# Kernel tuning notes

Hardware: AMD Instinct MI355X
Metric: run time of the kernel (lower is better)

## Reference

```python
import jax, jax.numpy as jnp
import numpy as np

H = 16          # n_heads
WIN = 256       # window_size
NEG_INF = -1e30 # finite stand-in for -inf to stay fp16/bf16 safe


def setup_inputs() -> dict:
    key = jax.random.key(0)
    ks = jax.random.split(key, 9)
    B, L, C = 2, 2048, 2048
    s = 0.02  # weight init scale
    inp = {
        "x": jax.random.normal(ks[0], (B, L, C), jnp.float32),
        "Wq": jax.random.normal(ks[1], (C, C), jnp.float32) * s,
        "bq": jnp.zeros((C,), jnp.float32),
        "Wk": jax.random.normal(ks[2], (C, C), jnp.float32) * s,
        "bk": jnp.zeros((C,), jnp.float32),
        "Wv": jax.random.normal(ks[3], (C, C), jnp.float32) * s,
        "bv": jnp.zeros((C,), jnp.float32),
        "Wo": jax.random.normal(ks[4], (C, C), jnp.float32) * s,
        "bo": jnp.zeros((C,), jnp.float32),
    }
    return inp


def _attn(x, Wq, bq, Wk, bk, Wv, bv, Wo, bo):
    B, L, C = x.shape
    D = C // H
    # torch Linear: y = x @ W.T + b
    q = (x @ Wq.T + bq).reshape(B, L, H, D).transpose(0, 2, 1, 3)  # (B,H,L,D)
    k = (x @ Wk.T + bk).reshape(B, L, H, D).transpose(0, 2, 1, 3)
    v = (x @ Wv.T + bv).reshape(B, L, H, D).transpose(0, 2, 1, 3)
    i = jnp.arange(L)[:, None]
    j = jnp.arange(L)[None, :]
    allowed = (j <= i) & (j > i - WIN)
    bias = jnp.where(allowed, 0.0, NEG_INF).astype(x.dtype)  # (L,L)
    scale = 1.0 / np.sqrt(D)
    attn = jnp.einsum('bhid,bhjd->bhij', q, k) + bias
    a = jax.nn.softmax(attn * scale, axis=-1)
    out = jnp.einsum('bhij,bhjd->bhid', a, v)  # (B,H,L,D)
    out = out.transpose(0, 2, 1, 3).reshape(B, L, C)
    return out @ Wo.T + bo  # dropout = identity (eval mode)


def reference(x, Wq, bq, Wk, bk, Wv, bv, Wo, bo):
    return _attn(x, Wq, bq, Wk, bk, Wv, bv, Wo, bo)
```

## Files before the change

### kernel.cpp

```cpp
#include <hip/hip_runtime.h>
#include <hip/hip_bf16.h>
#include <stdint.h>

typedef __bf16 bf16;
typedef __attribute__((ext_vector_type(8))) __bf16 bf16x8;
typedef __attribute__((ext_vector_type(8))) unsigned short u16x8;
typedef __attribute__((ext_vector_type(4))) float f32x4;

#define L_SEQ 2048
#define C_DIM 2048
#define NBATCH 2
#define M_ROWS (NBATCH * L_SEQ)
#define DH 128
#define NHEAD 16
#define WINSZ 256

__device__ __forceinline__ float san(float v, float s) {
    return ((__float_as_uint(v) & 0x7f800000u) == 0x7f800000u) ? s : v;
}

__device__ __forceinline__ bf16x8 pack8(float4 lo, float4 hi) {
    bf16x8 v;
    v[0] = (bf16)lo.x; v[1] = (bf16)lo.y; v[2] = (bf16)lo.z; v[3] = (bf16)lo.w;
    v[4] = (bf16)hi.x; v[5] = (bf16)hi.y; v[6] = (bf16)hi.z; v[7] = (bf16)hi.w;
    return v;
}

typedef const __attribute__((address_space(1))) void g_void;
typedef __attribute__((address_space(3))) void l_void;
__device__ __forceinline__ void glds16(const void* g, void* l) {
    __builtin_amdgcn_global_load_lds((g_void*)g, (l_void*)l, 16, 0, 0);
}

template <bool AF32, bool OUTF32>
__global__ __launch_bounds__(256)
void gemm_bt_bias(const void* __restrict__ Ap,
                  const float* __restrict__ W0, const float* __restrict__ b0, void* O0,
                  const float* __restrict__ W1, const float* __restrict__ b1, void* O1,
                  const float* __restrict__ W2, const float* __restrict__ b2, void* O2,
                  float snt)
{
    const int K = C_DIM, N = C_DIM;
    const float* W = W0; const float* bias = b0; void* Out = O0;
    if (blockIdx.z == 1)      { W = W1; bias = b1; Out = O1; }
    else if (blockIdx.z == 2) { W = W2; bias = b2; Out = O2; }

    __shared__ bf16 As[128 * 32];
    __shared__ bf16 Bs[128 * 32];

    const int tid  = threadIdx.x;
    const int lane = tid & 63;
    const int m0 = blockIdx.x * 128;
    const int n0 = blockIdx.y * 128;

    const int wave = tid >> 6;
    const int wm = (wave >> 1) * 64;
    const int wn = (wave & 1) * 64;

    const int srow = tid >> 2;
    const int scol = (tid & 3) * 8;

    f32x4 acc[4][4] = {};

    const int fr = lane & 15;
    const int fq = (lane >> 4) * 8;

    for (int k0 = 0; k0 < K; k0 += 32) {
        bf16x8 ra[2], rb[2];
        #pragma unroll
        for (int p = 0; p < 2; p++) {
            const size_t aoff = (size_t)(m0 + p * 64 + srow) * K + k0 + scol;
            if (AF32) {
                const float* A = (const float*)Ap;
                float4 lo = *(const float4*)(A + aoff);
                float4 hi = *(const float4*)(A + aoff + 4);
                ra[p] = pack8(lo, hi);
            } else {
                const bf16* A = (const bf16*)Ap;
                ra[p] = *(const bf16x8*)(A + aoff);
            }
            const size_t boff = (size_t)(n0 + p * 64 + srow) * K + k0 + scol;
            float4 wlo = *(const float4*)(W + boff);
            float4 whi = *(const float4*)(W + boff + 4);
            rb[p] = pack8(wlo, whi);
        }
        __syncthreads();
        #pragma unroll
        for (int p = 0; p < 2; p++) {
            *(bf16x8*)&As[(p * 64 + srow) * 32 + scol] = ra[p];
            *(bf16x8*)&Bs[(p * 64 + srow) * 32 + scol] = rb[p];
        }
        __syncthreads();

        bf16x8 af[4], bfr[4];
        #pragma unroll
        for (int s = 0; s < 4; s++)
            af[s] = *(const bf16x8*)&As[(wm + s * 16 + fr) * 32 + fq];
        #pragma unroll
        for (int s = 0; s < 4; s++)
            bfr[s] = *(const bf16x8*)&Bs[(wn + s * 16 + fr) * 32 + fq];
        #pragma unroll
        for (int sm = 0; sm < 4; sm++)
            #pragma unroll
            for (int sn = 0; sn < 4; sn++)
                acc[sm][sn] = __builtin_amdgcn_mfma_f32_16x16x32_bf16(af[sm], bfr[sn], acc[sm][sn], 0, 0, 0);
    }

    const int r0 = (lane >> 4) * 4;
    const int cn = lane & 15;
    #pragma unroll
    for (int sn = 0; sn < 4; sn++) {
        const int n = n0 + wn + sn * 16 + cn;
        const float bv = bias[n];
        #pragma unroll
        for (int sm = 0; sm < 4; sm++) {
            const int m = m0 + wm + sm * 16 + r0;
            #pragma unroll
            for (int r = 0; r < 4; r++) {
                const float v = san(acc[sm][sn][r] + bv, snt);
                if (OUTF32) ((float*)Out)[(size_t)(m + r) * N + n] = v;
                else        ((bf16*)Out)[(size_t)(m + r) * N + n] = (bf16)v;
            }
        }
    }
}

__device__ __forceinline__ void phase_mid() {
    asm volatile("" ::: "memory");
    __builtin_amdgcn_s_barrier();
    asm volatile("s_waitcnt lgkmcnt(0)" ::: "memory");
    __builtin_amdgcn_sched_barrier(0);
    __builtin_amdgcn_s_setprio(1);
}
__device__ __forceinline__ void phase_end() {
    __builtin_amdgcn_s_setprio(0);
    asm volatile("" ::: "memory");
    __builtin_amdgcn_s_barrier();
}

#define LOADA(d, qm) do {                                                     \
    char* s_ = lds + (d) * 65536 + ahalf * 16384;                             \
    _Pragma("unroll") for (int sm = 0; sm < 4; sm++)                          \
    _Pragma("unroll") for (int kk = 0; kk < 2; kk++) {                        \
        const int row_ = (qm) * 64 + sm * 16 + fr;                            \
        afr[sm][kk] = *(const bf16x8*)(s_ + row_ * 128 +                      \
                        (((kk * 4 + g) ^ (row_ & 7)) << 4));                  \
    } } while (0)

#define LOADB(d, qn, arr) do {                                                \
    char* s_ = lds + (d) * 65536 + 32768 + bhalf * 16384;                     \
    _Pragma("unroll") for (int sn = 0; sn < 2; sn++)                          \
    _Pragma("unroll") for (int kk = 0; kk < 2; kk++) {                        \
        const int row_ = brow0 + (qn) * 32 + sn * 16 + fr;                    \
        arr[sn][kk] = *(const bf16x8*)(s_ + row_ * 128 +                      \
                        (((kk * 4 + g) ^ (row_ & 7)) << 4));                  \
    } } while (0)

#define MFMA16(qm, qn, arr) do {                                              \
    _Pragma("unroll") for (int kk = 0; kk < 2; kk++)                          \
    _Pragma("unroll") for (int sm = 0; sm < 4; sm++)                          \
    _Pragma("unroll") for (int sn = 0; sn < 2; sn++)                          \
        acc[(qm) * 4 + sm][(qn) * 2 + sn] =                                   \
            __builtin_amdgcn_mfma_f32_16x16x32_bf16(afr[sm][kk], arr[sn][kk], \
                acc[(qm) * 4 + sm][(qn) * 2 + sn], 0, 0, 0);                  \
    } while (0)

template <bool OUTF32>
__global__ __launch_bounds__(512, 2)
void gemm_256(const bf16* __restrict__ A,
              const bf16* __restrict__ W0, const float* __restrict__ b0, void* O0,
              const bf16* __restrict__ W1, const float* __restrict__ b1, void* O1,
              const bf16* __restrict__ W2, const float* __restrict__ b2, void* O2,
              float snt)
{
    const int K = C_DIM, N = C_DIM;
    const int NT = K / 64;
    const bf16* W = W0; const float* bias = b0; void* Out = O0;
    if (blockIdx.z == 1)      { W = W1; bias = b1; Out = O1; }
    else if (blockIdx.z == 2) { W = W2; bias = b2; Out = O2; }

    __shared__ __attribute__((aligned(16))) char lds[131072];

    const int tid  = threadIdx.x;
    const int lane = tid & 63;
    const int w    = tid >> 6;

    int id = blockIdx.x + (int)gridDim.x * blockIdx.y;
    id = (id & 7) * 16 + (id >> 3);
    const int m0 = (id & 15) * 256;
    const int n0 = (id >> 4) * 256;

    const int wm = (w >> 2) * 128;
    const int wn = (w & 3) * 64;
    const int fr = lane & 15;
    const int g  = lane >> 4;
    const int ahalf = w >> 2;
    const int bhalf = (w >> 1) & 1;
    const int brow0 = (w & 1) * 64;

    const int srow  = tid >> 3;
    const int scol  = (((tid & 7) ^ (srow & 7)) * 8);
    const int wvoff = (tid >> 6) * 1024;

    f32x4 acc[8][4] = {};
    bf16x8 afr[4][2], b0r[2][2], b1r[2][2];

    #define STAGE_A(t, h) do {                                                \
        const int d_ = (t) & 1;                                               \
        const int tc_ = (t) < NT ? (t) : NT - 1;                              \
        const bf16* src_ = A + (size_t)(m0 + (h) * 128 + srow) * K            \
                             + tc_ * 64 + scol;                               \
        char* dst_ = lds + d_ * 65536 + (h) * 16384 + wvoff;                  \
        glds16(src_, dst_);                                                   \
        glds16(src_ + (size_t)64 * K, dst_ + 8192);                           \
    } while (0)

    #define STAGE_B(t, h) do {                                                \
        const int d_ = (t) & 1;                                               \
        const int tc_ = (t) < NT ? (t) : NT - 1;                              \
        const bf16* src_ = W + (size_t)(n0 + (h) * 128 + srow) * K            \
                             + tc_ * 64 + scol;                               \
        char* dst_ = lds + d_ * 65536 + 32768 + (h) * 16384 + wvoff;          \
        glds16(src_, dst_);                                                   \
        glds16(src_ + (size_t)64 * K, dst_ + 8192);                           \
    } while (0)

    STAGE_B(0, 0); STAGE_B(0, 1); STAGE_A(0, 0); STAGE_A(0, 1);
    STAGE_B(1, 0); STAGE_B(1, 1);
    asm volatile("s_waitcnt vmcnt(4)" ::: "memory");
    asm volatile("" ::: "memory");
    __builtin_amdgcn_s_barrier();

    #pragma unroll 1
    for (int i = 0; i < NT / 2; i++) {
        const int t1 = 2 * i + 1, t2 = 2 * i + 2, t3 = 2 * i + 3;
        LOADA(0, 0); LOADB(0, 0, b0r);
        STAGE_A(t1, 0);
        phase_mid(); MFMA16(0, 0, b0r); phase_end();
        LOADB(0, 1, b1r);
        STAGE_A(t1, 1);
        phase_mid(); MFMA16(0, 1, b1r); phase_end();
        LOADA(0, 1);
        STAGE_B(t2, 0);
        phase_mid(); MFMA16(1, 1, b1r); phase_end();
        STAGE_B(t2, 1);
        asm volatile("s_waitcnt vmcnt(4)" ::: "memory");
        phase_mid(); MFMA16(1, 0, b0r); phase_end();
        LOADA(1, 0); LOADB(1, 0, b0r);
        STAGE_A(t2, 0);
        phase_mid(); MFMA16(0, 0, b0r); phase_end();
        LOADB(1, 1, b1r);
        STAGE_A(t2, 1);
        phase_mid(); MFMA16(0, 1, b1r); phase_end();
        LOADA(1, 1);
        STAGE_B(t3, 0);
        phase_mid(); MFMA16(1, 1, b1r); phase_end();
        STAGE_B(t3, 1);
        asm volatile("s_waitcnt vmcnt(4)" ::: "memory");
        phase_mid(); MFMA16(1, 0, b0r); phase_end();
    }
    asm volatile("s_waitcnt vmcnt(0)" ::: "memory");

    const int cn = lane & 15;
    const int r0 = (lane >> 4) * 4;
    #pragma unroll
    for (int sn2 = 0; sn2 < 4; sn2++) {
        const int n = n0 + wn + sn2 * 16 + cn;
        const float bv = bias[n];
        #pragma unroll
        for (int sm2 = 0; sm2 < 8; sm2++) {
            const int m = m0 + wm + sm2 * 16 + r0;
            #pragma unroll
            for (int r = 0; r < 4; r++) {
                const float v = san(acc[sm2][sn2][r] + bv, snt);
                if (OUTF32) ((float*)Out)[(size_t)(m + r) * N + n] = v;
                else        ((bf16*)Out)[(size_t)(m + r) * N + n] = (bf16)v;
            }
        }
    }
    #undef STAGE_A
    #undef STAGE_B
}

__global__ __launch_bounds__(256)
void cvt_f32_bf16(const float* __restrict__ s0, bf16* __restrict__ d0,
                  const float* __restrict__ s1, bf16* __restrict__ d1,
                  const float* __restrict__ s2, bf16* __restrict__ d2,
                  const float* __restrict__ s3, bf16* __restrict__ d3,
                  const float* __restrict__ s4, bf16* __restrict__ d4)
{
    const float* s; bf16* d; int n;
    switch (blockIdx.y) {
        case 0:  s = s0; d = d0; n = M_ROWS * C_DIM; break;
        case 1:  s = s1; d = d1; n = C_DIM * C_DIM; break;
        case 2:  s = s2; d = d2; n = C_DIM * C_DIM; break;
        case 3:  s = s3; d = d3; n = C_DIM * C_DIM; break;
        default: s = s4; d = d4; n = C_DIM * C_DIM; break;
    }
    const int nv = n >> 3;
    const int stride = (int)gridDim.x * 256;
    for (int i = blockIdx.x * 256 + threadIdx.x; i < nv; i += stride) {
        const float4 lo = *(const float4*)(s + (size_t)i * 8);
        const float4 hi = *(const float4*)(s + (size_t)i * 8 + 4);
        *(bf16x8*)(d + (size_t)i * 8) = pack8(lo, hi);
    }
}

#define SWZK(r, byteoff) ((((r) * 256) + (byteoff)) ^ (((r) & 7) << 4))
#define SWZV(d, byteoff) ((((d) * 128) + (byteoff)) ^ (((((d) & 7) ^ (((d) >> 3) & 7))) << 4))
#define SWZP(r, byteoff) ((((r) * 128) + (byteoff)) ^ (((r) & 7) << 4))

__global__ __launch_bounds__(256)
void swa_attn(const bf16* __restrict__ Q, const bf16* __restrict__ Kp,
              const bf16* __restrict__ V, bf16* __restrict__ Oattn, float snt)
{
    __shared__ bf16 Ks[64 * 128];
    __shared__ bf16 Vt[128 * 64];
    __shared__ bf16 Ps[64 * 64];

    const int tid  = threadIdx.x;
    const int lane = tid & 63;
    const int w    = tid >> 6;
    const int q0 = blockIdx.x * 64;
    const int h  = blockIdx.y;
    const int b  = blockIdx.z;
    const size_t base = (size_t)b * L_SEQ * C_DIM + (size_t)h * DH;

    const int fr  = lane & 15;
    const int g   = lane >> 4;
    const int fq8 = g * 8;

    bf16x8 qf[4];
    {
        const bf16* qrow = Q + base + (size_t)(q0 + w * 16 + fr) * C_DIM;
        #pragma unroll
        for (int kk = 0; kk < 4; kk++)
            qf[kk] = *(const bf16x8*)(qrow + kk * 32 + fq8);
    }

    const int rl0 = g * 4;
    const int ig  = q0 + w * 16 + rl0;
    const float scale = 0.08838834764831845f;

    float m_run[4], l_run[4];
    #pragma unroll
    for (int r = 0; r < 4; r++) { m_run[r] = -1e30f; l_run[r] = 0.0f; }
    f32x4 Oacc[8] = {};

    const int krr = tid >> 4;
    const int kcc = (tid & 15) * 8;
    const int vc  = tid & 15;
    const int vd0 = vc * 8;
    const int vpb = tid >> 4;

    for (int kb = 0; kb < 5; kb++) {
        const int s = q0 - 256 + kb * 64;
        if (s < 0) continue;

        __syncthreads();

        #pragma unroll
        for (int p = 0; p < 4; p++) {
            const int r = p * 16 + krr;
            const uint4 kv = *(const uint4*)(Kp + base + (size_t)(s + r) * C_DIM + kcc);
            *(uint4*)((char*)Ks + SWZK(r, kcc * 2)) = kv;
        }
        #pragma unroll
        for (int it = 0; it < 2; it++) {
            const int p = vpb + it * 16;
            const bf16* vr = V + base + (size_t)(s + 2 * p) * C_DIM + vd0;
            const u16x8 va = *(const u16x8*)vr;
            const u16x8 vb = *(const u16x8*)(vr + C_DIM);
            #pragma unroll
            for (int j = 0; j < 8; j++) {
                const uint32_t val = (uint32_t)va[j] | ((uint32_t)vb[j] << 16);
                *(uint32_t*)((char*)Vt + SWZV(vd0 + j, 4 * p)) = val;
            }
        }
        __syncthreads();

        f32x4 sacc[4] = {};
        __builtin_amdgcn_s_setprio(1);
        #pragma unroll
        for (int kk = 0; kk < 4; kk++) {
            #pragma unroll
            for (int t = 0; t < 4; t++) {
                const bf16x8 kf = *(const bf16x8*)((char*)Ks + SWZK(t * 16 + fr, (kk * 32 + fq8) * 2));
                sacc[t] = __builtin_amdgcn_mfma_f32_16x16x32_bf16(qf[kk], kf, sacc[t], 0, 0, 0);
            }
        }
        __builtin_amdgcn_s_setprio(0);

        float alpha[4];
        #pragma unroll
        for (int r = 0; r < 4; r++) {
            const int iq = ig + r;
            float p4[4];
            float bm = -1e30f;
            #pragma unroll
            for (int t = 0; t < 4; t++) {
                const int j = s + t * 16 + fr;
                const bool allow = (j <= iq) && (j > iq - WINSZ);
                p4[t] = allow ? sacc[t][r] * scale : -1e30f;
                bm = fmaxf(bm, p4[t]);
            }
            bm = fmaxf(bm, __shfl_xor(bm, 1, 64));
            bm = fmaxf(bm, __shfl_xor(bm, 2, 64));
            bm = fmaxf(bm, __shfl_xor(bm, 4, 64));
            bm = fmaxf(bm, __shfl_xor(bm, 8, 64));
            const float m_new = fmaxf(m_run[r], bm);
            alpha[r] = __expf(m_run[r] - m_new);
            m_run[r] = m_new;
            float ps = 0.0f;
            #pragma unroll
            for (int t = 0; t < 4; t++) {
                const float e = (p4[t] > -1e29f) ? __expf(p4[t] - m_new) : 0.0f;
                p4[t] = e;
                ps += e;
            }
            ps += __shfl_xor(ps, 1, 64);
            ps += __shfl_xor(ps, 2, 64);
            ps += __shfl_xor(ps, 4, 64);
            ps += __shfl_xor(ps, 8, 64);
            l_run[r] = l_run[r] * alpha[r] + ps;

            const int prow = w * 16 + rl0 + r;
            #pragma unroll
            for (int t = 0; t < 4; t++)
                *(bf16*)((char*)Ps + SWZP(prow, (t * 16 + fr) * 2)) = (bf16)p4[t];
        }

        #pragma unroll
        for (int t = 0; t < 8; t++)
            #pragma unroll
            for (int r = 0; r < 4; r++)
                Oacc[t][r] *= alpha[r];

        __builtin_amdgcn_s_setprio(1);
        #pragma unroll
        for (int kk = 0; kk < 2; kk++) {
            const bf16x8 pa = *(const bf16x8*)((char*)Ps + SWZP(w * 16 + fr, (kk * 32 + fq8) * 2));
            #pragma unroll
            for (int t = 0; t < 8; t++) {
                const bf16x8 vf = *(const bf16x8*)((char*)Vt + SWZV(t * 16 + fr, (kk * 32 + fq8) * 2));
                Oacc[t] = __builtin_amdgcn_mfma_f32_16x16x32_bf16(pa, vf, Oacc[t], 0, 0, 0);
            }
        }
        __builtin_amdgcn_s_setprio(0);
    }

    bf16* ob = Oattn + base;
    #pragma unroll
    for (int r = 0; r < 4; r++) {
        const float inv_l = 1.0f / l_run[r];
        const size_t ro = (size_t)(q0 + w * 16 + rl0 + r) * C_DIM;
        #pragma unroll
        for (int t = 0; t < 8; t++)
            ob[ro + t * 16 + fr] = (bf16)san(Oacc[t][r] * inv_l, snt);
    }
}

__global__ void fill_signal(float* out, int n, float v) {
    for (int i = blockIdx.x * blockDim.x + threadIdx.x; i < n; i += gridDim.x * blockDim.x)
        out[i] = v;
}

extern "C" void kernel_launch(void* const* d_in, const int* in_sizes, int n_in,
                              void* d_out, int out_size, void* d_ws, size_t ws_size,
                              hipStream_t stream) {
    const size_t sz      = (size_t)M_ROWS * C_DIM;
    const size_t wsz     = (size_t)C_DIM * C_DIM;
    const size_t bfbytes = sz * sizeof(bf16);
    const size_t FASTNEED = 3 * sz * sizeof(bf16) + 4 * wsz * sizeof(bf16);

    const int expn[9] = {8388608, 4194304, 2048, 4194304, 2048,
                         4194304, 2048, 4194304, 2048};
    float sig = 0.0f;
    if (n_in != 9) sig = 1100.0f;
    else {
        for (int i = 0; i < 9; i++)
            if (in_sizes[i] != expn[i]) { sig = 1200.0f + 100.0f * i; break; }
    }
    if (sig == 0.0f && out_size != (int)sz) sig = 2100.0f;
    if (sig == 0.0f && ws_size < 2 * bfbytes) sig = 3000.0f + 10.0f * (float)(ws_size >> 20);
    if (sig != 0.0f) {
        fill_signal<<<512, 256, 0, stream>>>((float*)d_out, (int)sz, sig);
        return;
    }

    const float* x  = (const float*)d_in[0];
    const float* Wq = (const float*)d_in[1];
    const float* bq = (const float*)d_in[2];
    const float* Wk = (const float*)d_in[3];
    const float* bk = (const float*)d_in[4];
    const float* Wv = (const float*)d_in[5];
    const float* bv = (const float*)d_in[6];
    const float* Wo = (const float*)d_in[7];
    const float* bo = (const float*)d_in[8];

    if (ws_size >= FASTNEED) {
        bf16* xbf = (bf16*)d_ws;
        bf16* kws = xbf + sz;
        bf16* vws = kws + sz;
        bf16* wqb = vws + sz;
        bf16* wkb = wqb + wsz;
        bf16* wvb = wkb + wsz;
        bf16* wob = wvb + wsz;
        bf16*  qscr  = (bf16*)d_out;
        float* out32 = (float*)d_out;

        cvt_f32_bf16<<<dim3(2048, 5), 256, 0, stream>>>(
            x, xbf, Wq, wqb, Wk, wkb, Wv, wvb, Wo, wob);

        gemm_256<false><<<dim3(16, 8, 3), 512, 0, stream>>>(
            xbf, wqb, bq, (void*)qscr, wkb, bk, (void*)kws,
            wvb, bv, (void*)vws, 111.0f);

        swa_attn<<<dim3(L_SEQ / 64, NHEAD, NBATCH), 256, 0, stream>>>(
            qscr, kws, vws, xbf, 222.0f);

        gemm_256<true><<<dim3(16, 8, 1), 512, 0, stream>>>(
            xbf, wob, bo, (void*)out32, wob, bo, (void*)out32,
            wob, bo, (void*)out32, 444.0f);
    } else {
        bf16*  kws   = (bf16*)d_ws;
        bf16*  vws   = kws + sz;
        bf16*  qscr  = (bf16*)d_out;
        float* out32 = (float*)d_out;

        gemm_bt_bias<true, false><<<dim3(32, 16, 3), 256, 0, stream>>>(
            (const void*)x, Wq, bq, (void*)qscr, Wk, bk, (void*)kws,
            Wv, bv, (void*)vws, 111.0f);

        swa_attn<<<dim3(L_SEQ / 64, NHEAD, NBATCH), 256, 0, stream>>>(
            qscr, kws, vws, qscr, 222.0f);

        hipMemcpyAsync(kws, qscr, bfbytes, hipMemcpyDeviceToDevice, stream);

        gemm_bt_bias<false, true><<<dim3(32, 16, 1), 256, 0, stream>>>(
            (const void*)kws, Wo, bo, (void*)out32, Wo, bo, (void*)out32,
            Wo, bo, (void*)out32, 444.0f);
    }
}
```

Before: 359.8 us.

## Shrink GEMM block tile to 256x128 to double the grid and cut LDS

```diff
diff --git a/kernel.cpp b/kernel.cpp
--- a/kernel.cpp
+++ b/kernel.cpp
@@ -138,40 +138,43 @@
     __builtin_amdgcn_s_barrier();
 }
 
-#define LOADA(d, qm) do {                                                     \
-    char* s_ = lds + (d) * 65536 + ahalf * 16384;                             \
+#define BUFSZ 49152
+#define BOFF  32768
+
+#define LDA2(d) do {                                                          \
+    char* s_ = lds + (d) * BUFSZ + ahalf * 16384;                             \
     _Pragma("unroll") for (int sm = 0; sm < 4; sm++)                          \
     _Pragma("unroll") for (int kk = 0; kk < 2; kk++) {                        \
-        const int row_ = (qm) * 64 + sm * 16 + fr;                            \
+        const int row_ = arow0 + sm * 16 + fr;                                \
         afr[sm][kk] = *(const bf16x8*)(s_ + row_ * 128 +                      \
                         (((kk * 4 + g) ^ (row_ & 7)) << 4));                  \
     } } while (0)
 
-#define LOADB(d, qn, arr) do {                                                \
-    char* s_ = lds + (d) * 65536 + 32768 + bhalf * 16384;                     \
+#define LDB2(d, qn, arr) do {                                                 \
+    char* s_ = lds + (d) * BUFSZ + BOFF;                                      \
     _Pragma("unroll") for (int sn = 0; sn < 2; sn++)                          \
     _Pragma("unroll") for (int kk = 0; kk < 2; kk++) {                        \
-        const int row_ = brow0 + (qn) * 32 + sn * 16 + fr;                    \
+        const int row_ = wn + (qn) * 32 + sn * 16 + fr;                       \
         arr[sn][kk] = *(const bf16x8*)(s_ + row_ * 128 +                      \
                         (((kk * 4 + g) ^ (row_ & 7)) << 4));                  \
     } } while (0)
 
-#define MFMA16(qm, qn, arr) do {                                              \
+#define MFMAH(qn, arr) do {                                                   \
     _Pragma("unroll") for (int kk = 0; kk < 2; kk++)                          \
     _Pragma("unroll") for (int sm = 0; sm < 4; sm++)                          \
     _Pragma("unroll") for (int sn = 0; sn < 2; sn++)                          \
-        acc[(qm) * 4 + sm][(qn) * 2 + sn] =                                   \
+        acc[sm][(qn) * 2 + sn] =                                              \
             __builtin_amdgcn_mfma_f32_16x16x32_bf16(afr[sm][kk], arr[sn][kk], \
-                acc[(qm) * 4 + sm][(qn) * 2 + sn], 0, 0, 0);                  \
+                acc[sm][(qn) * 2 + sn], 0, 0, 0);                             \
     } while (0)
 
 template <bool OUTF32>
 __global__ __launch_bounds__(512, 2)
-void gemm_256(const bf16* __restrict__ A,
-              const bf16* __restrict__ W0, const float* __restrict__ b0, void* O0,
-              const bf16* __restrict__ W1, const float* __restrict__ b1, void* O1,
-              const bf16* __restrict__ W2, const float* __restrict__ b2, void* O2,
-              float snt)
+void gemm_256x128(const bf16* __restrict__ A,
+                  const bf16* __restrict__ W0, const float* __restrict__ b0, void* O0,
+                  const bf16* __restrict__ W1, const float* __restrict__ b1, void* O1,
+                  const bf16* __restrict__ W2, const float* __restrict__ b2, void* O2,
+                  float snt)
 {
     const int K = C_DIM, N = C_DIM;
     const int NT = K / 64;
@@ -179,54 +182,52 @@
     if (blockIdx.z == 1)      { W = W1; bias = b1; Out = O1; }
     else if (blockIdx.z == 2) { W = W2; bias = b2; Out = O2; }
 
-    __shared__ __attribute__((aligned(16))) char lds[131072];
+    __shared__ __attribute__((aligned(16))) char lds[98304];
 
     const int tid  = threadIdx.x;
     const int lane = tid & 63;
     const int w    = tid >> 6;
 
     int id = blockIdx.x + (int)gridDim.x * blockIdx.y;
-    id = (id & 7) * 16 + (id >> 3);
+    id = (id & 7) * 32 + (id >> 3);
     const int m0 = (id & 15) * 256;
-    const int n0 = (id >> 4) * 256;
-
-    const int wm = (w >> 2) * 128;
-    const int wn = (w & 3) * 64;
+    const int n0 = (id >> 4) * 128;
+
+    const int wm = (w >> 1) * 64;
+    const int wn = (w & 1) * 64;
     const int fr = lane & 15;
     const int g  = lane >> 4;
     const int ahalf = w >> 2;
-    const int bhalf = (w >> 1) & 1;
-    const int brow0 = (w & 1) * 64;
+    const int arow0 = ((w >> 1) & 1) * 64;
 
     const int srow  = tid >> 3;
     const int scol  = (((tid & 7) ^ (srow & 7)) * 8);
     const int wvoff = (tid >> 6) * 1024;
 
-    f32x4 acc[8][4] = {};
+    f32x4 acc[4][4] = {};
     bf16x8 afr[4][2], b0r[2][2], b1r[2][2];
 
-    #define STAGE_A(t, h) do {                                                \
+    #define STAGE_A(t) do {                                                   \
         const int d_ = (t) & 1;                                               \
         const int tc_ = (t) < NT ? (t) : NT - 1;                              \
-        const bf16* src_ = A + (size_t)(m0 + (h) * 128 + srow) * K            \
-                             + tc_ * 64 + scol;                               \
-        char* dst_ = lds + d_ * 65536 + (h) * 16384 + wvoff;                  \
-        glds16(src_, dst_);                                                   \
+        const bf16* src_ = A + (size_t)(m0 + srow) * K + tc_ * 64 + scol;     \
+        char* dst_ = lds + d_ * BUFSZ + wvoff;                                \
+        glds16(src_,                   dst_);                                 \
+        glds16(src_ + (size_t)64 * K,  dst_ + 8192);                          \
+        glds16(src_ + (size_t)128 * K, dst_ + 16384);                         \
+        glds16(src_ + (size_t)192 * K, dst_ + 24576);                         \
+    } while (0)
+
+    #define STAGE_B(t) do {                                                   \
+        const int d_ = (t) & 1;                                               \
+        const int tc_ = (t) < NT ? (t) : NT - 1;                              \
+        const bf16* src_ = W + (size_t)(n0 + srow) * K + tc_ * 64 + scol;     \
+        char* dst_ = lds + d_ * BUFSZ + BOFF + wvoff;                         \
+        glds16(src_,                  dst_);                                  \
         glds16(src_ + (size_t)64 * K, dst_ + 8192);                           \
     } while (0)
 
-    #define STAGE_B(t, h) do {                                                \
-        const int d_ = (t) & 1;                                               \
-        const int tc_ = (t) < NT ? (t) : NT - 1;                              \
-        const bf16* src_ = W + (size_t)(n0 + (h) * 128 + srow) * K            \
-                             + tc_ * 64 + scol;                               \
-        char* dst_ = lds + d_ * 65536 + 32768 + (h) * 16384 + wvoff;          \
-        glds16(src_, dst_);                                                   \
-        glds16(src_ + (size_t)64 * K, dst_ + 8192);                           \
-    } while (0)
-
-    STAGE_B(0, 0); STAGE_B(0, 1); STAGE_A(0, 0); STAGE_A(0, 1);
-    STAGE_B(1, 0); STAGE_B(1, 1);
+    STAGE_A(0); STAGE_B(0); STAGE_A(1);
     asm volatile("s_waitcnt vmcnt(4)" ::: "memory");
     asm volatile("" ::: "memory");
     __builtin_amdgcn_s_barrier();
@@ -234,30 +235,20 @@
     #pragma unroll 1
     for (int i = 0; i < NT / 2; i++) {
         const int t1 = 2 * i + 1, t2 = 2 * i + 2, t3 = 2 * i + 3;
-        LOADA(0, 0); LOADB(0, 0, b0r);
-        STAGE_A(t1, 0);
-        phase_mid(); MFMA16(0, 0, b0r); phase_end();
-        LOADB(0, 1, b1r);
-        STAGE_A(t1, 1);
-        phase_mid(); MFMA16(0, 1, b1r); phase_end();
-        LOADA(0, 1);
-        STAGE_B(t2, 0);
-        phase_mid(); MFMA16(1, 1, b1r); phase_end();
-        STAGE_B(t2, 1);
+        LDA2(0); LDB2(0, 0, b0r);
+        STAGE_B(t1);
+        phase_mid(); MFMAH(0, b0r); phase_end();
+        LDB2(0, 1, b1r);
+        STAGE_A(t2);
         asm volatile("s_waitcnt vmcnt(4)" ::: "memory");
-        phase_mid(); MFMA16(1, 0, b0r); phase_end();
-        LOADA(1, 0); LOADB(1, 0, b0r);
-        STAGE_A(t2, 0);
-        phase_mid(); MFMA16(0, 0, b0r); phase_end();
-        LOADB(1, 1, b1r);
-        STAGE_A(t2, 1);
-        phase_mid(); MFMA16(0, 1, b1r); phase_end();
-        LOADA(1, 1);
-        STAGE_B(t3, 0);
-        phase_mid(); MFMA16(1, 1, b1r); phase_end();
-        STAGE_B(t3, 1);
+        phase_mid(); MFMAH(1, b1r); phase_end();
+        LDA2(1); LDB2(1, 0, b0r);
+        STAGE_B(t2);
+        phase_mid(); MFMAH(0, b0r); phase_end();
+        LDB2(1, 1, b1r);
+        STAGE_A(t3);
         asm volatile("s_waitcnt vmcnt(4)" ::: "memory");
-        phase_mid(); MFMA16(1, 0, b0r); phase_end();
+        phase_mid(); MFMAH(1, b1r); phase_end();
     }
     asm volatile("s_waitcnt vmcnt(0)" ::: "memory");
 
@@ -268,7 +259,7 @@
         const int n = n0 + wn + sn2 * 16 + cn;
         const float bv = bias[n];
         #pragma unroll
-        for (int sm2 = 0; sm2 < 8; sm2++) {
+        for (int sm2 = 0; sm2 < 4; sm2++) {
             const int m = m0 + wm + sm2 * 16 + r0;
             #pragma unroll
             for (int r = 0; r < 4; r++) {
@@ -512,14 +503,14 @@
         cvt_f32_bf16<<<dim3(2048, 5), 256, 0, stream>>>(
             x, xbf, Wq, wqb, Wk, wkb, Wv, wvb, Wo, wob);
 
-        gemm_256<false><<<dim3(16, 8, 3), 512, 0, stream>>>(
+        gemm_256x128<false><<<dim3(16, 16, 3), 512, 0, stream>>>(
             xbf, wqb, bq, (void*)qscr, wkb, bk, (void*)kws,
             wvb, bv, (void*)vws, 111.0f);
 
         swa_attn<<<dim3(L_SEQ / 64, NHEAD, NBATCH), 256, 0, stream>>>(
             qscr, kws, vws, xbf, 222.0f);
 
-        gemm_256<true><<<dim3(16, 8, 1), 512, 0, stream>>>(
+        gemm_256x128<true><<<dim3(16, 16, 1), 512, 0, stream>>>(
             xbf, wob, bo, (void*)out32, wob, bo, (void*)out32,
             wob, bo, (void*)out32, 444.0f);
     } else {
```

Measured after the change: 329.5 us. -8.4%, faster.
